# Kernel optimization log

Hardware: AMD Instinct MI355X
Metric: run time of the kernel (lower is better)

The kernel has to match this reference:

```python
import jax, jax.numpy as jnp
import numpy as np
from jax import lax

N = 262144      # number of coordinate points
CC = 3          # coords_channel
GF = 64         # gating_feature
FEAT = 64       # n_network_features
E = 8           # experts_num
L = 4           # expert_layers
TOPK = 2
BW = 45.0       # bandwidth
LN_EPS = 1e-5
W0S = 0.5 * BW + BW * np.arange(E, dtype=np.float32)  # per-expert first-layer sine freq


def setup_inputs() -> dict:
    key = jax.random.key(0)
    ks = jax.random.split(key, 16)
    u = lambda k, shape, b: jax.random.uniform(k, shape, jnp.float32, -b, b)
    coords = jax.random.normal(ks[0], (N, CC), jnp.float32)
    # first_linear (first_layer_sine_init: U(-1/in, 1/in))
    fw = u(ks[1], (GF, CC), 1.0 / CC)
    fb = u(ks[2], (GF,), 1.0 / CC)
    # gate: Linear(GF,GF) + LayerNorm(GF), Linear(GF,E), softmax
    gw1 = u(ks[3], (GF, GF), np.sqrt(6.0 / GF))
    gb1 = u(ks[4], (GF,), 1.0 / np.sqrt(GF))
    ln_g = jnp.ones((GF,), jnp.float32)
    ln_b = jnp.zeros((GF,), jnp.float32)
    gw2 = u(ks[5], (E, GF), np.sqrt(6.0 / GF))
    gb2 = u(ks[6], (E,), 1.0 / np.sqrt(GF))
    # experts (SIREN): first layer U(-1/in,1/in), rest U(-sqrt(6/in)/30, sqrt(6/in)/30)
    we0 = u(ks[7], (E, FEAT, GF), 1.0 / GF)
    be0 = u(ks[8], (E, FEAT), 1.0 / GF)
    sb = np.sqrt(6.0 / FEAT) / 30.0
    wm = u(ks[9], (L - 2, E, FEAT, FEAT), sb)
    bm = u(ks[10], (L - 2, E, FEAT), sb)
    wl = u(ks[11], (E, FEAT), sb)
    bl = u(ks[12], (E,), sb)
    return {"coords": coords, "fw": fw, "fb": fb, "gw1": gw1, "gb1": gb1,
            "ln_g": ln_g, "ln_b": ln_b, "gw2": gw2, "gb2": gb2,
            "we0": we0, "be0": be0, "wm": wm, "bm": bm, "wl": wl, "bl": bl}


def reference(coords, fw, fb, gw1, gb1, ln_g, ln_b, gw2, gb2, we0, be0, wm, bm, wl, bl):
    w0s = jnp.asarray(W0S)
    # first_linear: [N, GF]
    feature = coords @ fw.T + fb
    # gate: Linear -> LayerNorm -> Linear -> Softmax(dim=1)
    g = feature @ gw1.T + gb1
    mu = jnp.mean(g, axis=-1, keepdims=True)
    var = jnp.mean(jnp.square(g - mu), axis=-1, keepdims=True)
    gn = (g - mu) * lax.rsqrt(var + LN_EPS) * ln_g + ln_b
    index = jax.nn.softmax(gn @ gw2.T + gb2, axis=1)  # [N, E]
    # all experts computed densely on the gated feature: [E, N, FEAT]
    h = jnp.sin(w0s[:, None, None] * (jnp.einsum('nf,ekf->enk', feature, we0) + be0[:, None, :]))
    for l in range(L - 2):
        h = jnp.sin(30.0 * (jnp.einsum('enf,ekf->enk', h, wm[l]) + bm[l][:, None, :]))
    x = (jnp.einsum('enf,ef->en', h, wl) + bl[:, None]).T  # [N, E]
    # top-k mask: ~(index < kth largest) == index >= kth
    kth = lax.top_k(index, TOPK)[0][:, -1:]
    mask = (index >= kth).astype(x.dtype)
    output = jnp.sum(x * mask, axis=1, keepdims=True)  # [N, 1]
    counts = jnp.sum(mask, axis=0)  # per-expert selection counts
    aux_loss = (E / (N * N)) * jnp.dot(counts, counts)
    return output, aux_loss
```

## Files before the change

kernel.cpp:

```cpp
#include <hip/hip_runtime.h>
#include <math.h>

#define NPTS 262144
#define GBLK (NPTS / 128)
#define CPE  2048
#define TAU  0.01f

typedef float f4v __attribute__((ext_vector_type(4)));
typedef short s8v __attribute__((ext_vector_type(8)));

static __device__ __forceinline__ unsigned short f2bf(float f) {
    unsigned u = __float_as_uint(f);
    u += 0x7fffu + ((u >> 16) & 1u);
    return (unsigned short)(u >> 16);
}
static __device__ __forceinline__ unsigned short f2bf_hw(float f) {
    __bf16 b = (__bf16)f;
    unsigned short u;
    __builtin_memcpy(&u, &b, 2);
    return u;
}
static __device__ __forceinline__ float bf2f(unsigned short h) {
    return __uint_as_float(((unsigned)h) << 16);
}
static __device__ __forceinline__ unsigned pk2b(unsigned short lo, unsigned short hi) {
    return ((unsigned)hi << 16) | (unsigned)lo;
}
static __device__ __forceinline__ unsigned cpack(float lo, float hi) {
    return pk2b(f2bf_hw(lo), f2bf_hw(hi));
}
static __device__ __forceinline__ float sinrev(float x) {
    return __builtin_amdgcn_sinf(x);
}

union BFrag { uint4 q; unsigned u[4]; s8v s; };

__global__ __launch_bounds__(256) void prep_kernel(
    const float* __restrict__ we0, const float* __restrict__ be0,
    const float* __restrict__ wm, const float* __restrict__ bm,
    const float* __restrict__ gw1, const float* __restrict__ gw2,
    const float* __restrict__ fw, const float* __restrict__ fb,
    const float* __restrict__ gb1,
    uint4* __restrict__ packA, float* __restrict__ biasS,
    uint4* __restrict__ packGW2H, uint4* __restrict__ packGW2L,
    float* __restrict__ M1, float* __restrict__ b1p,
    float* __restrict__ M0, float* __restrict__ b0p, int* __restrict__ refcnt)
{
    const int idx = blockIdx.x * 256 + threadIdx.x;
    const float PI2I = 0.15915494309189535f;
    if (idx < 12288) {
        const int l = idx & 63;
        const int fr = (idx >> 6) & 7;
        const int grp = idx >> 9;
        const int e = grp / 3, ell = grp % 3;
        const int tau = fr >> 1, ks = fr & 1;
        const int g = l >> 4, m = l & 15;
        const int row = tau * 16 + m;
        const float scale = (ell == 0) ? (22.5f + 45.0f * (float)e) * PI2I : 30.0f * PI2I;
        const float* W = (ell == 0) ? (we0 + e * 4096) : (wm + ((ell - 1) * 8 + e) * 4096);
        unsigned short v[8];
#pragma unroll
        for (int i = 0; i < 8; i++) {
            const int k = 32 * ks + 4 * g + (i < 4 ? i : i + 12);
            v[i] = f2bf(W[row * 64 + k] * scale);
        }
        uint4 q;
        q.x = pk2b(v[0], v[1]); q.y = pk2b(v[2], v[3]);
        q.z = pk2b(v[4], v[5]); q.w = pk2b(v[6], v[7]);
        packA[idx] = q;
    } else if (idx < 13824) {
        const int j = idx - 12288;
        const int r = j & 63;
        const int grp = j >> 6;
        const int e = grp / 3, ell = grp % 3;
        const float scale = (ell == 0) ? (22.5f + 45.0f * (float)e) * PI2I : 30.0f * PI2I;
        const float b = (ell == 0) ? be0[e * 64 + r] : bm[((ell - 1) * 8 + e) * 64 + r];
        biasS[j] = b * scale;
    } else if (idx < 13952) {
        const int j = idx - 13824;
        const int l = j & 63;
        const int ks = j >> 6;
        const int g = l >> 4;
        const int row = l & 15;
        unsigned short vh[8], vl[8];
#pragma unroll
        for (int i = 0; i < 8; i++) {
            const int k = 32 * ks + 4 * g + (i < 4 ? i : i + 12);
            const float x = (row < 8) ? gw2[row * 64 + k] : 0.f;
            const unsigned short h = f2bf(x);
            vh[i] = h;
            vl[i] = f2bf(x - bf2f(h));
        }
        uint4 qh, ql;
        qh.x = pk2b(vh[0], vh[1]); qh.y = pk2b(vh[2], vh[3]);
        qh.z = pk2b(vh[4], vh[5]); qh.w = pk2b(vh[6], vh[7]);
        ql.x = pk2b(vl[0], vl[1]); ql.y = pk2b(vl[2], vl[3]);
        ql.z = pk2b(vl[4], vl[5]); ql.w = pk2b(vl[6], vl[7]);
        packGW2H[j] = qh; packGW2L[j] = ql;
    } else if (idx < 14144) {
        const int m = idx - 13952;
        const int r = m / 3, d = m % 3;
        double s = 0.0;
        for (int j = 0; j < 64; j++) s += (double)gw1[r * 64 + j] * (double)fw[j * 3 + d];
        M1[m] = (float)s;
    } else if (idx < 14208) {
        const int r = idx - 14144;
        double s = (double)gb1[r];
        for (int j = 0; j < 64; j++) s += (double)gw1[r * 64 + j] * (double)fb[j];
        b1p[r] = (float)s;
    } else if (idx < 15744) {
        const int m = idx - 14208;
        const int e = m / 192;
        const int rem = m % 192;
        const int r = rem / 3, d = rem % 3;
        const double scale = (22.5 + 45.0 * (double)e) * 0.15915494309189535;
        double s = 0.0;
        for (int j = 0; j < 64; j++) s += (double)we0[e * 4096 + r * 64 + j] * (double)fw[j * 3 + d];
        M0[m] = (float)(s * scale);
    } else if (idx < 16256) {
        const int m = idx - 15744;
        const int e = m >> 6, r = m & 63;
        const double scale = (22.5 + 45.0 * (double)e) * 0.15915494309189535;
        double s = (double)be0[e * 64 + r];
        for (int j = 0; j < 64; j++) s += (double)we0[e * 4096 + r * 64 + j] * (double)fb[j];
        b0p[m] = (float)(s * scale);
    } else if (idx == 16256) {
        *refcnt = 0;
    }
}

__global__ __launch_bounds__(256) void gate_kernel(
    const float* __restrict__ coords,
    const float* __restrict__ M1, const float* __restrict__ b1p,
    const float* __restrict__ lng, const float* __restrict__ lnb,
    const float* __restrict__ gb2,
    const uint4* __restrict__ packGW2H, const uint4* __restrict__ packGW2L,
    unsigned char* __restrict__ sel, int* __restrict__ blkcnt,
    int* __restrict__ reflist, int* __restrict__ refcnt, float* __restrict__ out)
{
    __shared__ float s_M1[192], s_b1p[64], s_lng[64], s_lnb[64], s_gb2[8];
    __shared__ uint4 sW2H[128], sW2L[128];
    __shared__ int s_cnt[8];
    const int t = threadIdx.x;
    if (t < 128) { sW2H[t] = packGW2H[t]; sW2L[t] = packGW2L[t]; }
    if (t < 192) s_M1[t] = M1[t];
    if (t < 64) { s_b1p[t] = b1p[t]; s_lng[t] = lng[t]; s_lnb[t] = lnb[t]; }
    if (t < 8) { s_gb2[t] = gb2[t]; s_cnt[t] = 0; }
    if (t < 128) out[blockIdx.x * 128 + t] = 0.f;
    __syncthreads();

    const int lane = t & 63;
    const int wv = t >> 6;
    const int g = lane >> 4, c = lane & 15;
    const int n0 = blockIdx.x * 128 + wv * 32 + c;
    const int n1 = n0 + 16;

    const float a0 = coords[n0 * 3], a1 = coords[n0 * 3 + 1], a2 = coords[n0 * 3 + 2];
    const float b0 = coords[n1 * 3], b1 = coords[n1 * 3 + 1], b2 = coords[n1 * 3 + 2];

    float ga[16], gb[16];
#pragma unroll
    for (int i = 0; i < 16; i++) {
        const int r = ((i >> 2) << 4) + 4 * g + (i & 3);
        const float m0 = s_M1[r * 3], m1 = s_M1[r * 3 + 1], m2 = s_M1[r * 3 + 2];
        const float bb = s_b1p[r];
        ga[i] = bb + a0 * m0 + a1 * m1 + a2 * m2;
        gb[i] = bb + b0 * m0 + b1 * m1 + b2 * m2;
    }

    float s1a = 0.f, s1b = 0.f;
#pragma unroll
    for (int i = 0; i < 16; i++) { s1a += ga[i]; s1b += gb[i]; }
    s1a += __shfl_xor(s1a, 16, 64); s1a += __shfl_xor(s1a, 32, 64);
    s1b += __shfl_xor(s1b, 16, 64); s1b += __shfl_xor(s1b, 32, 64);
    const float mu0 = s1a * (1.f / 64.f), mu1 = s1b * (1.f / 64.f);
    float s2a = 0.f, s2b = 0.f;
#pragma unroll
    for (int i = 0; i < 16; i++) {
        const float d0 = ga[i] - mu0; s2a += d0 * d0;
        const float d1 = gb[i] - mu1; s2b += d1 * d1;
    }
    s2a += __shfl_xor(s2a, 16, 64); s2a += __shfl_xor(s2a, 32, 64);
    s2b += __shfl_xor(s2b, 16, 64); s2b += __shfl_xor(s2b, 32, 64);
    const float rs0 = rsqrtf(s2a * (1.f / 64.f) + 1e-5f);
    const float rs1 = rsqrtf(s2b * (1.f / 64.f) + 1e-5f);

    BFrag Gh0[2], Gl0[2], Gh1[2], Gl1[2];
#pragma unroll
    for (int ks = 0; ks < 2; ks++) {
#pragma unroll
        for (int q = 0; q < 4; q++) {
            const int i0 = ks * 8 + 2 * q, i1 = i0 + 1;
            const int r0 = ((i0 >> 2) << 4) + 4 * g + (i0 & 3);
            const int r1 = ((i1 >> 2) << 4) + 4 * g + (i1 & 3);
            const float gnA0 = (ga[i0] - mu0) * rs0 * s_lng[r0] + s_lnb[r0];
            const float gnA1 = (ga[i1] - mu0) * rs0 * s_lng[r1] + s_lnb[r1];
            const float gnB0 = (gb[i0] - mu1) * rs1 * s_lng[r0] + s_lnb[r0];
            const float gnB1 = (gb[i1] - mu1) * rs1 * s_lng[r1] + s_lnb[r1];
            const unsigned short hA0 = f2bf_hw(gnA0), hA1 = f2bf_hw(gnA1);
            const unsigned short hB0 = f2bf_hw(gnB0), hB1 = f2bf_hw(gnB1);
            Gh0[ks].u[q] = pk2b(hA0, hA1);
            Gl0[ks].u[q] = cpack(gnA0 - bf2f(hA0), gnA1 - bf2f(hA1));
            Gh1[ks].u[q] = pk2b(hB0, hB1);
            Gl1[ks].u[q] = cpack(gnB0 - bf2f(hB0), gnB1 - bf2f(hB1));
        }
    }

    f4v lacc0 = {0.f, 0.f, 0.f, 0.f}, lacc1 = {0.f, 0.f, 0.f, 0.f};
    {
        BFrag W0, W1, V0, V1;
        W0.q = sW2H[0 * 64 + lane]; W1.q = sW2H[1 * 64 + lane];
        V0.q = sW2L[0 * 64 + lane]; V1.q = sW2L[1 * 64 + lane];
        lacc0 = __builtin_amdgcn_mfma_f32_16x16x32_bf16(W0.s, Gh0[0].s, lacc0, 0, 0, 0);
        lacc1 = __builtin_amdgcn_mfma_f32_16x16x32_bf16(W0.s, Gh1[0].s, lacc1, 0, 0, 0);
        lacc0 = __builtin_amdgcn_mfma_f32_16x16x32_bf16(W1.s, Gh0[1].s, lacc0, 0, 0, 0);
        lacc1 = __builtin_amdgcn_mfma_f32_16x16x32_bf16(W1.s, Gh1[1].s, lacc1, 0, 0, 0);
        lacc0 = __builtin_amdgcn_mfma_f32_16x16x32_bf16(W0.s, Gl0[0].s, lacc0, 0, 0, 0);
        lacc1 = __builtin_amdgcn_mfma_f32_16x16x32_bf16(W0.s, Gl1[0].s, lacc1, 0, 0, 0);
        lacc0 = __builtin_amdgcn_mfma_f32_16x16x32_bf16(W1.s, Gl0[1].s, lacc0, 0, 0, 0);
        lacc1 = __builtin_amdgcn_mfma_f32_16x16x32_bf16(W1.s, Gl1[1].s, lacc1, 0, 0, 0);
        lacc0 = __builtin_amdgcn_mfma_f32_16x16x32_bf16(V0.s, Gh0[0].s, lacc0, 0, 0, 0);
        lacc1 = __builtin_amdgcn_mfma_f32_16x16x32_bf16(V0.s, Gh1[0].s, lacc1, 0, 0, 0);
        lacc0 = __builtin_amdgcn_mfma_f32_16x16x32_bf16(V1.s, Gh0[1].s, lacc0, 0, 0, 0);
        lacc1 = __builtin_amdgcn_mfma_f32_16x16x32_bf16(V1.s, Gh1[1].s, lacc1, 0, 0, 0);
    }

    float logit0[8], logit1[8];
#pragma unroll
    for (int j = 0; j < 4; j++) {
        const float o0 = __shfl_xor(lacc0[j], 16, 64);
        const float o1 = __shfl_xor(lacc1[j], 16, 64);
        logit0[j] = lacc0[j] + s_gb2[j];
        logit0[4 + j] = o0 + s_gb2[4 + j];
        logit1[j] = lacc1[j] + s_gb2[j];
        logit1[4 + j] = o1 + s_gb2[4 + j];
    }

    unsigned mbits0 = 0, mbits1 = 0;
    bool flg0, flg1;
    {
        float m1 = logit0[0]; int i1 = 0;
#pragma unroll
        for (int e = 1; e < 8; e++) if (logit0[e] > m1) { m1 = logit0[e]; i1 = e; }
        float m2 = -INFINITY; int i2 = -1;
#pragma unroll
        for (int e = 0; e < 8; e++) if (e != i1 && logit0[e] > m2) { m2 = logit0[e]; i2 = e; }
        float m3 = -INFINITY;
#pragma unroll
        for (int e = 0; e < 8; e++) if (e != i1 && e != i2 && logit0[e] > m3) m3 = logit0[e];
#pragma unroll
        for (int e = 0; e < 8; e++) if (logit0[e] >= m2) mbits0 |= 1u << e;
        flg0 = (m2 - m3 < TAU);
    }
    {
        float m1 = logit1[0]; int i1 = 0;
#pragma unroll
        for (int e = 1; e < 8; e++) if (logit1[e] > m1) { m1 = logit1[e]; i1 = e; }
        float m2 = -INFINITY; int i2 = -1;
#pragma unroll
        for (int e = 0; e < 8; e++) if (e != i1 && logit1[e] > m2) { m2 = logit1[e]; i2 = e; }
        float m3 = -INFINITY;
#pragma unroll
        for (int e = 0; e < 8; e++) if (e != i1 && e != i2 && logit1[e] > m3) m3 = logit1[e];
#pragma unroll
        for (int e = 0; e < 8; e++) if (logit1[e] >= m2) mbits1 |= 1u << e;
        flg1 = (m2 - m3 < TAU);
    }

    const bool active = (g == 0);
    if (active) { sel[n0] = (unsigned char)mbits0; sel[n1] = (unsigned char)mbits1; }

#pragma unroll
    for (int e = 0; e < 8; e++) {
        const unsigned long long bal0 = __ballot(active && ((mbits0 >> e) & 1u));
        const unsigned long long bal1 = __ballot(active && ((mbits1 >> e) & 1u));
        if (lane == 0) atomicAdd(&s_cnt[e], (int)(__popcll(bal0) + __popcll(bal1)));
    }
    {
        const unsigned long long bal0 = __ballot(active && flg0);
        const unsigned long long bal1 = __ballot(active && flg1);
        const int p0 = (int)__popcll(bal0);
        int pos0 = 0;
        if (lane == 0 && (bal0 | bal1)) pos0 = atomicAdd(refcnt, p0 + (int)__popcll(bal1));
        pos0 = __shfl(pos0, 0, 64);
        if (active && flg0) {
            const int rank = (int)__popcll(bal0 & ((1ull << lane) - 1ull));
            reflist[pos0 + rank] = n0;
        }
        if (active && flg1) {
            const int rank = p0 + (int)__popcll(bal1 & ((1ull << lane) - 1ull));
            reflist[pos0 + rank] = n1;
        }
    }
    __syncthreads();
    if (t < 8) blkcnt[blockIdx.x * 8 + t] = s_cnt[t];
}

__global__ __launch_bounds__(256) void refine_kernel(
    const float* __restrict__ coords,
    const float* __restrict__ fw, const float* __restrict__ fb,
    const float* __restrict__ gw1, const float* __restrict__ gb1,
    const float* __restrict__ lng, const float* __restrict__ lnb,
    const float* __restrict__ gw2, const float* __restrict__ gb2,
    const int* __restrict__ reflist, const int* __restrict__ refcnt,
    unsigned char* __restrict__ sel, int* __restrict__ blkcnt)
{
    const int R = *refcnt;
    if (blockIdx.x * 4 >= R) return;

    __shared__ float s_gw1t[64 * 65];
    __shared__ float s_gw2[512];
    __shared__ float s_fw[192], s_fb[64], s_gb1[64], s_lng[64], s_lnb[64], s_gb2[8];
    __shared__ float s_f[4][64];

    const int t = threadIdx.x;
    for (int i = t; i < 4096; i += 256) s_gw1t[(i & 63) * 65 + (i >> 6)] = gw1[i];
    for (int i = t; i < 512; i += 256) s_gw2[i] = gw2[i];
    if (t < 192) s_fw[t] = fw[t];
    if (t < 64) { s_fb[t] = fb[t]; s_gb1[t] = gb1[t]; s_lng[t] = lng[t]; s_lnb[t] = lnb[t]; }
    if (t < 8) s_gb2[t] = gb2[t];
    __syncthreads();

    const int wv = t >> 6, lane = t & 63;
    for (int idx = blockIdx.x * 4 + wv; idx < R; idx += gridDim.x * 4) {
        const int n = reflist[idx];
        const float c0 = coords[n * 3], c1 = coords[n * 3 + 1], c2 = coords[n * 3 + 2];
        const float fr = s_fb[lane] + c0 * s_fw[lane * 3] + c1 * s_fw[lane * 3 + 1]
                       + c2 * s_fw[lane * 3 + 2];
        s_f[wv][lane] = fr;
        float a = s_gb1[lane];
#pragma unroll
        for (int k = 0; k < 64; k++)
            a += s_f[wv][k] * s_gw1t[k * 65 + lane];
        float mu = a;
#pragma unroll
        for (int d = 1; d < 64; d <<= 1) mu += __shfl_xor(mu, d, 64);
        mu *= (1.f / 64.f);
        const float dv = a - mu;
        float v = dv * dv;
#pragma unroll
        for (int d = 1; d < 64; d <<= 1) v += __shfl_xor(v, d, 64);
        const float rs = rsqrtf(v * (1.f / 64.f) + 1e-5f);
        const float gn = dv * rs * s_lng[lane] + s_lnb[lane];
        float lp[8];
#pragma unroll
        for (int e = 0; e < 8; e++) lp[e] = gn * s_gw2[e * 64 + lane];
#pragma unroll
        for (int e = 0; e < 8; e++) {
#pragma unroll
            for (int d = 1; d < 64; d <<= 1) lp[e] += __shfl_xor(lp[e], d, 64);
            lp[e] += s_gb2[e];
        }
        if (lane == 0) {
            float m1 = lp[0]; int i1 = 0;
#pragma unroll
            for (int e = 1; e < 8; e++) if (lp[e] > m1) { m1 = lp[e]; i1 = e; }
            float m2 = -INFINITY;
#pragma unroll
            for (int e = 0; e < 8; e++) if (e != i1 && lp[e] > m2) m2 = lp[e];
            unsigned mbits = 0;
#pragma unroll
            for (int e = 0; e < 8; e++) if (lp[e] >= m2) mbits |= 1u << e;
            const unsigned old = sel[n];
            if (mbits != old) {
                sel[n] = (unsigned char)mbits;
                const int b = n >> 7;
#pragma unroll
                for (int e = 0; e < 8; e++) {
                    const int was = (old >> e) & 1, now = (mbits >> e) & 1;
                    if (was != now) atomicAdd(&blkcnt[b * 8 + e], now - was);
                }
            }
        }
    }
}

__global__ __launch_bounds__(256) void scan_kernel(
    const int* __restrict__ blkcnt, int* __restrict__ baseoff,
    int* __restrict__ counts)
{
    const int e = blockIdx.x;
    const int t = threadIdx.x;
    const int lane = t & 63, wv = t >> 6;
    __shared__ int s_w[4];

    int v[8]; int sum = 0;
#pragma unroll
    for (int i = 0; i < 8; i++) { v[i] = blkcnt[(t * 8 + i) * 8 + e]; sum += v[i]; }
    int incl = sum;
#pragma unroll
    for (int d = 1; d < 64; d <<= 1) {
        const int x = __shfl_up(incl, d, 64);
        if (lane >= d) incl += x;
    }
    if (lane == 63) s_w[wv] = incl;
    __syncthreads();
    int woff = 0;
#pragma unroll
    for (int i = 0; i < 4; i++) if (i < wv) woff += s_w[i];
    int run = woff + incl - sum;
#pragma unroll
    for (int i = 0; i < 8; i++) { baseoff[(t * 8 + i) * 8 + e] = run; run += v[i]; }
    if (t == 255) counts[e] = run;
}

__global__ __launch_bounds__(128) void scatter_kernel(
    const unsigned char* __restrict__ sel, const int* __restrict__ baseoff,
    const int* __restrict__ counts, int* __restrict__ buckets, float* __restrict__ out)
{
    __shared__ int s_w0[8];
    const int t = threadIdx.x;
    const int n = blockIdx.x * 128 + t;
    if (blockIdx.x == 0 && t == 0) {
        double s = 0.0;
        for (int e = 0; e < 8; e++) { const double c = (double)counts[e]; s += c * c; }
        out[NPTS] = (float)(8.0 * s / ((double)NPTS * (double)NPTS));
    }
    const unsigned m = sel[n];
    const int w = t >> 6, lane = t & 63;
    unsigned long long bal[8];
#pragma unroll
    for (int e = 0; e < 8; e++) {
        bal[e] = __ballot((m >> e) & 1u);
        if (w == 0 && lane == 0) s_w0[e] = (int)__popcll(bal[e]);
    }
    __syncthreads();
#pragma unroll
    for (int e = 0; e < 8; e++) {
        if ((m >> e) & 1u) {
            int rank = (int)__popcll(bal[e] & ((1ull << lane) - 1ull));
            if (w == 1) rank += s_w0[e];
            buckets[e * NPTS + baseoff[blockIdx.x * 8 + e] + rank] = n;
        }
    }
}

__global__ __launch_bounds__(256) void expert_kernel(
    const float* __restrict__ coords,
    const float* __restrict__ M0, const float* __restrict__ b0p,
    const float* __restrict__ wl, const float* __restrict__ bl,
    const uint4* __restrict__ packA, const float* __restrict__ biasS,
    const int* __restrict__ counts, const int* __restrict__ buckets,
    float* __restrict__ out)
{
    const int e = blockIdx.x >> 11;
    const int chunk = blockIdx.x & (CPE - 1);
    const int cnt = counts[e];
    const int base = chunk * 128;
    if (base >= cnt) return;

    __shared__ float s_b[192];
    __shared__ float s_wl[64];
    __shared__ float s_M0[192];
    __shared__ float s_b0p[64];
    __shared__ float s_bl;

    const int t = threadIdx.x;
    if (t < 192) {
        s_b[t] = biasS[e * 192 + t];
        s_M0[t] = M0[e * 192 + t];
    }
    if (t < 64) {
        s_b0p[t] = b0p[e * 64 + t];
        s_wl[t] = wl[e * 64 + t];
    }
    if (t == 0) s_bl = bl[e];
    __syncthreads();

    const int lane = t & 63;
    const int wv = t >> 6;
    const int g = lane >> 4, c = lane & 15;
    const int i0 = base + wv * 32 + c;
    const int i1 = i0 + 16;
    const int id0 = (i0 < cnt) ? buckets[e * NPTS + i0] : -1;
    const int id1 = (i1 < cnt) ? buckets[e * NPTS + i1] : -1;

    const float a0 = (id0 >= 0) ? coords[id0 * 3] : 0.f;
    const float a1 = (id0 >= 0) ? coords[id0 * 3 + 1] : 0.f;
    const float a2 = (id0 >= 0) ? coords[id0 * 3 + 2] : 0.f;
    const float b0 = (id1 >= 0) ? coords[id1 * 3] : 0.f;
    const float b1 = (id1 >= 0) ? coords[id1 * 3 + 1] : 0.f;
    const float b2 = (id1 >= 0) ? coords[id1 * 3 + 2] : 0.f;

    f4v acc0[4], acc1[4];
#pragma unroll
    for (int tau = 0; tau < 4; tau++) {
#pragma unroll
        for (int j = 0; j < 4; j++) {
            const int r = tau * 16 + 4 * g + j;
            const float m0 = s_M0[r * 3], m1 = s_M0[r * 3 + 1], m2 = s_M0[r * 3 + 2];
            const float bb = s_b0p[r];
            acc0[tau][j] = bb + a0 * m0 + a1 * m1 + a2 * m2;
            acc1[tau][j] = bb + b0 * m0 + b1 * m1 + b2 * m2;
        }
    }

    BFrag B0[2], B1[2];
#pragma unroll
    for (int ks = 0; ks < 2; ks++) {
        B0[ks].u[0] = cpack(sinrev(acc0[2 * ks][0]), sinrev(acc0[2 * ks][1]));
        B0[ks].u[1] = cpack(sinrev(acc0[2 * ks][2]), sinrev(acc0[2 * ks][3]));
        B0[ks].u[2] = cpack(sinrev(acc0[2 * ks + 1][0]), sinrev(acc0[2 * ks + 1][1]));
        B0[ks].u[3] = cpack(sinrev(acc0[2 * ks + 1][2]), sinrev(acc0[2 * ks + 1][3]));
        B1[ks].u[0] = cpack(sinrev(acc1[2 * ks][0]), sinrev(acc1[2 * ks][1]));
        B1[ks].u[1] = cpack(sinrev(acc1[2 * ks][2]), sinrev(acc1[2 * ks][3]));
        B1[ks].u[2] = cpack(sinrev(acc1[2 * ks + 1][0]), sinrev(acc1[2 * ks + 1][1]));
        B1[ks].u[3] = cpack(sinrev(acc1[2 * ks + 1][2]), sinrev(acc1[2 * ks + 1][3]));
    }

    {
#pragma unroll
        for (int tau = 0; tau < 4; tau++) {
            const float4 b = *(const float4*)&s_b[64 + tau * 16 + 4 * g];
            acc0[tau][0] = b.x; acc0[tau][1] = b.y; acc0[tau][2] = b.z; acc0[tau][3] = b.w;
            acc1[tau][0] = b.x; acc1[tau][1] = b.y; acc1[tau][2] = b.z; acc1[tau][3] = b.w;
        }
        const uint4* Ab = packA + (size_t)((e * 3 + 1) * 8) * 64 + lane;
#pragma unroll
        for (int tau = 0; tau < 4; tau++) {
            BFrag A0, A1;
            A0.q = Ab[(tau * 2 + 0) * 64];
            A1.q = Ab[(tau * 2 + 1) * 64];
            acc0[tau] = __builtin_amdgcn_mfma_f32_16x16x32_bf16(A0.s, B0[0].s, acc0[tau], 0, 0, 0);
            acc0[tau] = __builtin_amdgcn_mfma_f32_16x16x32_bf16(A1.s, B0[1].s, acc0[tau], 0, 0, 0);
            acc1[tau] = __builtin_amdgcn_mfma_f32_16x16x32_bf16(A0.s, B1[0].s, acc1[tau], 0, 0, 0);
            acc1[tau] = __builtin_amdgcn_mfma_f32_16x16x32_bf16(A1.s, B1[1].s, acc1[tau], 0, 0, 0);
        }
#pragma unroll
        for (int ks = 0; ks < 2; ks++) {
            B0[ks].u[0] = cpack(sinrev(acc0[2 * ks][0]), sinrev(acc0[2 * ks][1]));
            B0[ks].u[1] = cpack(sinrev(acc0[2 * ks][2]), sinrev(acc0[2 * ks][3]));
            B0[ks].u[2] = cpack(sinrev(acc0[2 * ks + 1][0]), sinrev(acc0[2 * ks + 1][1]));
            B0[ks].u[3] = cpack(sinrev(acc0[2 * ks + 1][2]), sinrev(acc0[2 * ks + 1][3]));
            B1[ks].u[0] = cpack(sinrev(acc1[2 * ks][0]), sinrev(acc1[2 * ks][1]));
            B1[ks].u[1] = cpack(sinrev(acc1[2 * ks][2]), sinrev(acc1[2 * ks][3]));
            B1[ks].u[2] = cpack(sinrev(acc1[2 * ks + 1][0]), sinrev(acc1[2 * ks + 1][1]));
            B1[ks].u[3] = cpack(sinrev(acc1[2 * ks + 1][2]), sinrev(acc1[2 * ks + 1][3]));
        }
    }

    {
#pragma unroll
        for (int tau = 0; tau < 4; tau++) {
            const float4 b = *(const float4*)&s_b[128 + tau * 16 + 4 * g];
            acc0[tau][0] = b.x; acc0[tau][1] = b.y; acc0[tau][2] = b.z; acc0[tau][3] = b.w;
            acc1[tau][0] = b.x; acc1[tau][1] = b.y; acc1[tau][2] = b.z; acc1[tau][3] = b.w;
        }
        const uint4* Ab = packA + (size_t)((e * 3 + 2) * 8) * 64 + lane;
#pragma unroll
        for (int tau = 0; tau < 4; tau++) {
            BFrag A0, A1;
            A0.q = Ab[(tau * 2 + 0) * 64];
            A1.q = Ab[(tau * 2 + 1) * 64];
            acc0[tau] = __builtin_amdgcn_mfma_f32_16x16x32_bf16(A0.s, B0[0].s, acc0[tau], 0, 0, 0);
            acc0[tau] = __builtin_amdgcn_mfma_f32_16x16x32_bf16(A1.s, B0[1].s, acc0[tau], 0, 0, 0);
            acc1[tau] = __builtin_amdgcn_mfma_f32_16x16x32_bf16(A0.s, B1[0].s, acc1[tau], 0, 0, 0);
            acc1[tau] = __builtin_amdgcn_mfma_f32_16x16x32_bf16(A1.s, B1[1].s, acc1[tau], 0, 0, 0);
        }
        float px0 = 0.f, px1 = 0.f;
#pragma unroll
        for (int tau = 0; tau < 4; tau++) {
            const float4 w = *(const float4*)&s_wl[tau * 16 + 4 * g];
            px0 += sinrev(acc0[tau][0]) * w.x + sinrev(acc0[tau][1]) * w.y
                 + sinrev(acc0[tau][2]) * w.z + sinrev(acc0[tau][3]) * w.w;
            px1 += sinrev(acc1[tau][0]) * w.x + sinrev(acc1[tau][1]) * w.y
                 + sinrev(acc1[tau][2]) * w.z + sinrev(acc1[tau][3]) * w.w;
        }
        px0 += __shfl_xor(px0, 16, 64); px0 += __shfl_xor(px0, 32, 64);
        px1 += __shfl_xor(px1, 16, 64); px1 += __shfl_xor(px1, 32, 64);
        if (g == 0) {
            if (id0 >= 0) atomicAdd(&out[id0], px0 + s_bl);
            if (id1 >= 0) atomicAdd(&out[id1], px1 + s_bl);
        }
    }
}

extern "C" void kernel_launch(void* const* d_in, const int* in_sizes, int n_in,
                              void* d_out, int out_size, void* d_ws, size_t ws_size,
                              hipStream_t stream)
{
    const float* coords = (const float*)d_in[0];
    const float* fw  = (const float*)d_in[1];
    const float* fb  = (const float*)d_in[2];
    const float* gw1 = (const float*)d_in[3];
    const float* gb1 = (const float*)d_in[4];
    const float* lng = (const float*)d_in[5];
    const float* lnb = (const float*)d_in[6];
    const float* gw2 = (const float*)d_in[7];
    const float* gb2 = (const float*)d_in[8];
    const float* we0 = (const float*)d_in[9];
    const float* be0 = (const float*)d_in[10];
    const float* wm  = (const float*)d_in[11];
    const float* bm  = (const float*)d_in[12];
    const float* wl  = (const float*)d_in[13];
    const float* bl  = (const float*)d_in[14];
    float* out = (float*)d_out;

    char* ws = (char*)d_ws;
    int* counts           = (int*)ws;
    int* buckets          = (int*)(ws + 64);
    uint4* packA          = (uint4*)(ws + 8388672);
    float* biasS          = (float*)(ws + 8585280);
    int* blkcnt           = (int*)(ws + 8591424);
    int* baseoff          = (int*)(ws + 8656960);
    unsigned char* sel    = (unsigned char*)(ws + 8722496);
    uint4* packGW2H       = (uint4*)(ws + 8984640);
    uint4* packGW2L       = (uint4*)(ws + 8986688);
    int* reflist          = (int*)(ws + 8988736);
    int* refcnt           = (int*)(ws + 10037312);
    float* M1             = (float*)(ws + 10037376);
    float* b1p            = (float*)(ws + 10038144);
    float* M0             = (float*)(ws + 10038400);
    float* b0p            = (float*)(ws + 10044544);

    prep_kernel<<<64, 256, 0, stream>>>(we0, be0, wm, bm, gw1, gw2, fw, fb, gb1,
                                        packA, biasS, packGW2H, packGW2L, M1, b1p,
                                        M0, b0p, refcnt);
    gate_kernel<<<GBLK, 256, 0, stream>>>(coords, M1, b1p, lng, lnb, gb2,
                                          packGW2H, packGW2L,
                                          sel, blkcnt, reflist, refcnt, out);
    refine_kernel<<<256, 256, 0, stream>>>(coords, fw, fb, gw1, gb1, lng, lnb, gw2, gb2,
                                           reflist, refcnt, sel, blkcnt);
    scan_kernel<<<8, 256, 0, stream>>>(blkcnt, baseoff, counts);
    scatter_kernel<<<GBLK, 128, 0, stream>>>(sel, baseoff, counts, buckets, out);
    expert_kernel<<<8 * CPE, 256, 0, stream>>>(coords, M0, b0p, wl, bl, packA, biasS,
                                               counts, buckets, out);
}
```

Before: 85.77 us.

## Fuse scan into refine via last-block ticket; make expert kernel persistent

The per-expert prefix scan now runs inside the refine kernel, performed by whichever block finishes last (detected with an atomic ticket counter that prep resets). This removes one kernel launch. The expert kernel becomes a grid-stride loop over a compacted list of 128-point chunks across all experts, launched with 2056 blocks instead of 16384 mostly-empty ones. In exchange, each loop iteration reloads per-expert shared weights behind an extra barrier, and correctness depends on the threadfence/ticket ordering.

```diff
diff --git a/kernel.cpp b/kernel.cpp
--- a/kernel.cpp
+++ b/kernel.cpp
@@ -3,7 +3,6 @@
 
 #define NPTS 262144
 #define GBLK (NPTS / 128)
-#define CPE  2048
 #define TAU  0.01f
 
 typedef float f4v __attribute__((ext_vector_type(4)));
@@ -44,7 +43,8 @@
     uint4* __restrict__ packA, float* __restrict__ biasS,
     uint4* __restrict__ packGW2H, uint4* __restrict__ packGW2L,
     float* __restrict__ M1, float* __restrict__ b1p,
-    float* __restrict__ M0, float* __restrict__ b0p, int* __restrict__ refcnt)
+    float* __restrict__ M0, float* __restrict__ b0p,
+    int* __restrict__ refcnt, int* __restrict__ rs_done)
 {
     const int idx = blockIdx.x * 256 + threadIdx.x;
     const float PI2I = 0.15915494309189535f;
@@ -126,6 +126,8 @@
         b0p[m] = (float)(s * scale);
     } else if (idx == 16256) {
         *refcnt = 0;
+    } else if (idx == 16257) {
+        *rs_done = 0;
     }
 }
 
@@ -303,105 +305,109 @@
     const float* __restrict__ lng, const float* __restrict__ lnb,
     const float* __restrict__ gw2, const float* __restrict__ gb2,
     const int* __restrict__ reflist, const int* __restrict__ refcnt,
-    unsigned char* __restrict__ sel, int* __restrict__ blkcnt)
+    unsigned char* __restrict__ sel, int* __restrict__ blkcnt,
+    int* __restrict__ baseoff, int* __restrict__ counts, int* __restrict__ rs_done)
 {
-    const int R = *refcnt;
-    if (blockIdx.x * 4 >= R) return;
-
     __shared__ float s_gw1t[64 * 65];
     __shared__ float s_gw2[512];
     __shared__ float s_fw[192], s_fb[64], s_gb1[64], s_lng[64], s_lnb[64], s_gb2[8];
     __shared__ float s_f[4][64];
+    __shared__ int s_ticket;
+    __shared__ int s_wsc[4];
 
     const int t = threadIdx.x;
-    for (int i = t; i < 4096; i += 256) s_gw1t[(i & 63) * 65 + (i >> 6)] = gw1[i];
-    for (int i = t; i < 512; i += 256) s_gw2[i] = gw2[i];
-    if (t < 192) s_fw[t] = fw[t];
-    if (t < 64) { s_fb[t] = fb[t]; s_gb1[t] = gb1[t]; s_lng[t] = lng[t]; s_lnb[t] = lnb[t]; }
-    if (t < 8) s_gb2[t] = gb2[t];
+    const int wv = t >> 6, lane = t & 63;
+    const int R = *refcnt;
+
+    if (R > 0 && blockIdx.x * 4 < R) {
+        for (int i = t; i < 4096; i += 256) s_gw1t[(i & 63) * 65 + (i >> 6)] = gw1[i];
+        for (int i = t; i < 512; i += 256) s_gw2[i] = gw2[i];
+        if (t < 192) s_fw[t] = fw[t];
+        if (t < 64) { s_fb[t] = fb[t]; s_gb1[t] = gb1[t]; s_lng[t] = lng[t]; s_lnb[t] = lnb[t]; }
+        if (t < 8) s_gb2[t] = gb2[t];
+        __syncthreads();
+
+        for (int idx = blockIdx.x * 4 + wv; idx < R; idx += gridDim.x * 4) {
+            const int n = reflist[idx];
+            const float c0 = coords[n * 3], c1 = coords[n * 3 + 1], c2 = coords[n * 3 + 2];
+            const float fr = s_fb[lane] + c0 * s_fw[lane * 3] + c1 * s_fw[lane * 3 + 1]
+                           + c2 * s_fw[lane * 3 + 2];
+            s_f[wv][lane] = fr;
+            float a = s_gb1[lane];
+#pragma unroll
+            for (int k = 0; k < 64; k++)
+                a += s_f[wv][k] * s_gw1t[k * 65 + lane];
+            float mu = a;
+#pragma unroll
+            for (int d = 1; d < 64; d <<= 1) mu += __shfl_xor(mu, d, 64);
+            mu *= (1.f / 64.f);
+            const float dv = a - mu;
+            float v = dv * dv;
+#pragma unroll
+            for (int d = 1; d < 64; d <<= 1) v += __shfl_xor(v, d, 64);
+            const float rs = rsqrtf(v * (1.f / 64.f) + 1e-5f);
+            const float gn = dv * rs * s_lng[lane] + s_lnb[lane];
+            float lp[8];
+#pragma unroll
+            for (int e = 0; e < 8; e++) lp[e] = gn * s_gw2[e * 64 + lane];
+#pragma unroll
+            for (int e = 0; e < 8; e++) {
+#pragma unroll
+                for (int d = 1; d < 64; d <<= 1) lp[e] += __shfl_xor(lp[e], d, 64);
+                lp[e] += s_gb2[e];
+            }
+            if (lane == 0) {
+                float m1 = lp[0]; int i1 = 0;
+#pragma unroll
+                for (int e = 1; e < 8; e++) if (lp[e] > m1) { m1 = lp[e]; i1 = e; }
+                float m2 = -INFINITY;
+#pragma unroll
+                for (int e = 0; e < 8; e++) if (e != i1 && lp[e] > m2) m2 = lp[e];
+                unsigned mbits = 0;
+#pragma unroll
+                for (int e = 0; e < 8; e++) if (lp[e] >= m2) mbits |= 1u << e;
+                const unsigned old = sel[n];
+                if (mbits != old) {
+                    sel[n] = (unsigned char)mbits;
+                    const int b = n >> 7;
+#pragma unroll
+                    for (int e = 0; e < 8; e++) {
+                        const int was = (old >> e) & 1, now = (mbits >> e) & 1;
+                        if (was != now) atomicAdd(&blkcnt[b * 8 + e], now - was);
+                    }
+                }
+            }
+        }
+    }
+
+    __threadfence();
     __syncthreads();
-
-    const int wv = t >> 6, lane = t & 63;
-    for (int idx = blockIdx.x * 4 + wv; idx < R; idx += gridDim.x * 4) {
-        const int n = reflist[idx];
-        const float c0 = coords[n * 3], c1 = coords[n * 3 + 1], c2 = coords[n * 3 + 2];
-        const float fr = s_fb[lane] + c0 * s_fw[lane * 3] + c1 * s_fw[lane * 3 + 1]
-                       + c2 * s_fw[lane * 3 + 2];
-        s_f[wv][lane] = fr;
-        float a = s_gb1[lane];
-#pragma unroll
-        for (int k = 0; k < 64; k++)
-            a += s_f[wv][k] * s_gw1t[k * 65 + lane];
-        float mu = a;
-#pragma unroll
-        for (int d = 1; d < 64; d <<= 1) mu += __shfl_xor(mu, d, 64);
-        mu *= (1.f / 64.f);
-        const float dv = a - mu;
-        float v = dv * dv;
-#pragma unroll
-        for (int d = 1; d < 64; d <<= 1) v += __shfl_xor(v, d, 64);
-        const float rs = rsqrtf(v * (1.f / 64.f) + 1e-5f);
-        const float gn = dv * rs * s_lng[lane] + s_lnb[lane];
-        float lp[8];
-#pragma unroll
-        for (int e = 0; e < 8; e++) lp[e] = gn * s_gw2[e * 64 + lane];
-#pragma unroll
+    if (t == 0) s_ticket = atomicAdd(rs_done, 1);
+    __syncthreads();
+    if (s_ticket == (int)gridDim.x - 1) {
+        __threadfence();
         for (int e = 0; e < 8; e++) {
-#pragma unroll
-            for (int d = 1; d < 64; d <<= 1) lp[e] += __shfl_xor(lp[e], d, 64);
-            lp[e] += s_gb2[e];
-        }
-        if (lane == 0) {
-            float m1 = lp[0]; int i1 = 0;
-#pragma unroll
-            for (int e = 1; e < 8; e++) if (lp[e] > m1) { m1 = lp[e]; i1 = e; }
-            float m2 = -INFINITY;
-#pragma unroll
-            for (int e = 0; e < 8; e++) if (e != i1 && lp[e] > m2) m2 = lp[e];
-            unsigned mbits = 0;
-#pragma unroll
-            for (int e = 0; e < 8; e++) if (lp[e] >= m2) mbits |= 1u << e;
-            const unsigned old = sel[n];
-            if (mbits != old) {
-                sel[n] = (unsigned char)mbits;
-                const int b = n >> 7;
-#pragma unroll
-                for (int e = 0; e < 8; e++) {
-                    const int was = (old >> e) & 1, now = (mbits >> e) & 1;
-                    if (was != now) atomicAdd(&blkcnt[b * 8 + e], now - was);
-                }
-            }
-        }
-    }
-}
-
-__global__ __launch_bounds__(256) void scan_kernel(
-    const int* __restrict__ blkcnt, int* __restrict__ baseoff,
-    int* __restrict__ counts)
-{
-    const int e = blockIdx.x;
-    const int t = threadIdx.x;
-    const int lane = t & 63, wv = t >> 6;
-    __shared__ int s_w[4];
-
-    int v[8]; int sum = 0;
-#pragma unroll
-    for (int i = 0; i < 8; i++) { v[i] = blkcnt[(t * 8 + i) * 8 + e]; sum += v[i]; }
-    int incl = sum;
-#pragma unroll
-    for (int d = 1; d < 64; d <<= 1) {
-        const int x = __shfl_up(incl, d, 64);
-        if (lane >= d) incl += x;
-    }
-    if (lane == 63) s_w[wv] = incl;
-    __syncthreads();
-    int woff = 0;
-#pragma unroll
-    for (int i = 0; i < 4; i++) if (i < wv) woff += s_w[i];
-    int run = woff + incl - sum;
-#pragma unroll
-    for (int i = 0; i < 8; i++) { baseoff[(t * 8 + i) * 8 + e] = run; run += v[i]; }
-    if (t == 255) counts[e] = run;
+            int v[8]; int sum = 0;
+#pragma unroll
+            for (int i = 0; i < 8; i++) { v[i] = blkcnt[(t * 8 + i) * 8 + e]; sum += v[i]; }
+            int incl = sum;
+#pragma unroll
+            for (int d = 1; d < 64; d <<= 1) {
+                const int x = __shfl_up(incl, d, 64);
+                if (lane >= d) incl += x;
+            }
+            if (lane == 63) s_wsc[wv] = incl;
+            __syncthreads();
+            int woff = 0;
+#pragma unroll
+            for (int i = 0; i < 4; i++) if (i < wv) woff += s_wsc[i];
+            int run = woff + incl - sum;
+#pragma unroll
+            for (int i = 0; i < 8; i++) { baseoff[(t * 8 + i) * 8 + e] = run; run += v[i]; }
+            if (t == 255) counts[e] = run;
+            __syncthreads();
+        }
+    }
 }
 
 __global__ __launch_bounds__(128) void scatter_kernel(
@@ -443,12 +449,6 @@
     const int* __restrict__ counts, const int* __restrict__ buckets,
     float* __restrict__ out)
 {
-    const int e = blockIdx.x >> 11;
-    const int chunk = blockIdx.x & (CPE - 1);
-    const int cnt = counts[e];
-    const int base = chunk * 128;
-    if (base >= cnt) return;
-
     __shared__ float s_b[192];
     __shared__ float s_wl[64];
     __shared__ float s_M0[192];
@@ -456,76 +456,66 @@
     __shared__ float s_bl;
 
     const int t = threadIdx.x;
-    if (t < 192) {
-        s_b[t] = biasS[e * 192 + t];
-        s_M0[t] = M0[e * 192 + t];
-    }
-    if (t < 64) {
-        s_b0p[t] = b0p[e * 64 + t];
-        s_wl[t] = wl[e * 64 + t];
-    }
-    if (t == 0) s_bl = bl[e];
-    __syncthreads();
-
-    const int lane = t & 63;
-    const int wv = t >> 6;
-    const int g = lane >> 4, c = lane & 15;
-    const int i0 = base + wv * 32 + c;
-    const int i1 = i0 + 16;
-    const int id0 = (i0 < cnt) ? buckets[e * NPTS + i0] : -1;
-    const int id1 = (i1 < cnt) ? buckets[e * NPTS + i1] : -1;
-
-    const float a0 = (id0 >= 0) ? coords[id0 * 3] : 0.f;
-    const float a1 = (id0 >= 0) ? coords[id0 * 3 + 1] : 0.f;
-    const float a2 = (id0 >= 0) ? coords[id0 * 3 + 2] : 0.f;
-    const float b0 = (id1 >= 0) ? coords[id1 * 3] : 0.f;
-    const float b1 = (id1 >= 0) ? coords[id1 * 3 + 1] : 0.f;
-    const float b2 = (id1 >= 0) ? coords[id1 * 3 + 2] : 0.f;
-
-    f4v acc0[4], acc1[4];
-#pragma unroll
-    for (int tau = 0; tau < 4; tau++) {
-#pragma unroll
-        for (int j = 0; j < 4; j++) {
-            const int r = tau * 16 + 4 * g + j;
-            const float m0 = s_M0[r * 3], m1 = s_M0[r * 3 + 1], m2 = s_M0[r * 3 + 2];
-            const float bb = s_b0p[r];
-            acc0[tau][j] = bb + a0 * m0 + a1 * m1 + a2 * m2;
-            acc1[tau][j] = bb + b0 * m0 + b1 * m1 + b2 * m2;
-        }
-    }
-
-    BFrag B0[2], B1[2];
-#pragma unroll
-    for (int ks = 0; ks < 2; ks++) {
-        B0[ks].u[0] = cpack(sinrev(acc0[2 * ks][0]), sinrev(acc0[2 * ks][1]));
-        B0[ks].u[1] = cpack(sinrev(acc0[2 * ks][2]), sinrev(acc0[2 * ks][3]));
-        B0[ks].u[2] = cpack(sinrev(acc0[2 * ks + 1][0]), sinrev(acc0[2 * ks + 1][1]));
-        B0[ks].u[3] = cpack(sinrev(acc0[2 * ks + 1][2]), sinrev(acc0[2 * ks + 1][3]));
-        B1[ks].u[0] = cpack(sinrev(acc1[2 * ks][0]), sinrev(acc1[2 * ks][1]));
-        B1[ks].u[1] = cpack(sinrev(acc1[2 * ks][2]), sinrev(acc1[2 * ks][3]));
-        B1[ks].u[2] = cpack(sinrev(acc1[2 * ks + 1][0]), sinrev(acc1[2 * ks + 1][1]));
-        B1[ks].u[3] = cpack(sinrev(acc1[2 * ks + 1][2]), sinrev(acc1[2 * ks + 1][3]));
-    }
-
-    {
+    const int c0n = (counts[0] + 127) >> 7;
+    const int c1n = (counts[1] + 127) >> 7;
+    const int c2n = (counts[2] + 127) >> 7;
+    const int c3n = (counts[3] + 127) >> 7;
+    const int c4n = (counts[4] + 127) >> 7;
+    const int c5n = (counts[5] + 127) >> 7;
+    const int c6n = (counts[6] + 127) >> 7;
+    const int c7n = (counts[7] + 127) >> 7;
+    const int p1 = c0n, p2 = p1 + c1n, p3 = p2 + c2n, p4 = p3 + c3n;
+    const int p5 = p4 + c4n, p6 = p5 + c5n, p7 = p6 + c6n, total = p7 + c7n;
+
+    bool first = true;
+    for (int vc = blockIdx.x; vc < total; vc += gridDim.x) {
+        int e = 0, pe = 0;
+        if (vc >= p1) { e = 1; pe = p1; }
+        if (vc >= p2) { e = 2; pe = p2; }
+        if (vc >= p3) { e = 3; pe = p3; }
+        if (vc >= p4) { e = 4; pe = p4; }
+        if (vc >= p5) { e = 5; pe = p5; }
+        if (vc >= p6) { e = 6; pe = p6; }
+        if (vc >= p7) { e = 7; pe = p7; }
+        const int cnt = counts[e];
+        const int base = (vc - pe) * 128;
+
+        if (!first) __syncthreads();
+        first = false;
+        if (t < 192) { s_b[t] = biasS[e * 192 + t]; s_M0[t] = M0[e * 192 + t]; }
+        if (t < 64) { s_b0p[t] = b0p[e * 64 + t]; s_wl[t] = wl[e * 64 + t]; }
+        if (t == 0) s_bl = bl[e];
+        __syncthreads();
+
+        const int lane = t & 63;
+        const int wv = t >> 6;
+        const int g = lane >> 4, c = lane & 15;
+        const int i0 = base + wv * 32 + c;
+        const int i1 = i0 + 16;
+        const int id0 = (i0 < cnt) ? buckets[e * NPTS + i0] : -1;
+        const int id1 = (i1 < cnt) ? buckets[e * NPTS + i1] : -1;
+
+        const float a0 = (id0 >= 0) ? coords[id0 * 3] : 0.f;
+        const float a1 = (id0 >= 0) ? coords[id0 * 3 + 1] : 0.f;
+        const float a2 = (id0 >= 0) ? coords[id0 * 3 + 2] : 0.f;
+        const float b0 = (id1 >= 0) ? coords[id1 * 3] : 0.f;
+        const float b1 = (id1 >= 0) ? coords[id1 * 3 + 1] : 0.f;
+        const float b2 = (id1 >= 0) ? coords[id1 * 3 + 2] : 0.f;
+
+        f4v acc0[4], acc1[4];
 #pragma unroll
         for (int tau = 0; tau < 4; tau++) {
-            const float4 b = *(const float4*)&s_b[64 + tau * 16 + 4 * g];
-            acc0[tau][0] = b.x; acc0[tau][1] = b.y; acc0[tau][2] = b.z; acc0[tau][3] = b.w;
-            acc1[tau][0] = b.x; acc1[tau][1] = b.y; acc1[tau][2] = b.z; acc1[tau][3] = b.w;
-        }
-        const uint4* Ab = packA + (size_t)((e * 3 + 1) * 8) * 64 + lane;
-#pragma unroll
-        for (int tau = 0; tau < 4; tau++) {
-            BFrag A0, A1;
-            A0.q = Ab[(tau * 2 + 0) * 64];
-            A1.q = Ab[(tau * 2 + 1) * 64];
-            acc0[tau] = __builtin_amdgcn_mfma_f32_16x16x32_bf16(A0.s, B0[0].s, acc0[tau], 0, 0, 0);
-            acc0[tau] = __builtin_amdgcn_mfma_f32_16x16x32_bf16(A1.s, B0[1].s, acc0[tau], 0, 0, 0);
-            acc1[tau] = __builtin_amdgcn_mfma_f32_16x16x32_bf16(A0.s, B1[0].s, acc1[tau], 0, 0, 0);
-            acc1[tau] = __builtin_amdgcn_mfma_f32_16x16x32_bf16(A1.s, B1[1].s, acc1[tau], 0, 0, 0);
-        }
+#pragma unroll
+            for (int j = 0; j < 4; j++) {
+                const int r = tau * 16 + 4 * g + j;
+                const float m0 = s_M0[r * 3], m1 = s_M0[r * 3 + 1], m2 = s_M0[r * 3 + 2];
+                const float bb = s_b0p[r];
+                acc0[tau][j] = bb + a0 * m0 + a1 * m1 + a2 * m2;
+                acc1[tau][j] = bb + b0 * m0 + b1 * m1 + b2 * m2;
+            }
+        }
+
+        BFrag B0[2], B1[2];
 #pragma unroll
         for (int ks = 0; ks < 2; ks++) {
             B0[ks].u[0] = cpack(sinrev(acc0[2 * ks][0]), sinrev(acc0[2 * ks][1]));
@@ -537,40 +527,71 @@
             B1[ks].u[2] = cpack(sinrev(acc1[2 * ks + 1][0]), sinrev(acc1[2 * ks + 1][1]));
             B1[ks].u[3] = cpack(sinrev(acc1[2 * ks + 1][2]), sinrev(acc1[2 * ks + 1][3]));
         }
-    }
-
-    {
-#pragma unroll
-        for (int tau = 0; tau < 4; tau++) {
-            const float4 b = *(const float4*)&s_b[128 + tau * 16 + 4 * g];
-            acc0[tau][0] = b.x; acc0[tau][1] = b.y; acc0[tau][2] = b.z; acc0[tau][3] = b.w;
-            acc1[tau][0] = b.x; acc1[tau][1] = b.y; acc1[tau][2] = b.z; acc1[tau][3] = b.w;
-        }
-        const uint4* Ab = packA + (size_t)((e * 3 + 2) * 8) * 64 + lane;
-#pragma unroll
-        for (int tau = 0; tau < 4; tau++) {
-            BFrag A0, A1;
-            A0.q = Ab[(tau * 2 + 0) * 64];
-            A1.q = Ab[(tau * 2 + 1) * 64];
-            acc0[tau] = __builtin_amdgcn_mfma_f32_16x16x32_bf16(A0.s, B0[0].s, acc0[tau], 0, 0, 0);
-            acc0[tau] = __builtin_amdgcn_mfma_f32_16x16x32_bf16(A1.s, B0[1].s, acc0[tau], 0, 0, 0);
-            acc1[tau] = __builtin_amdgcn_mfma_f32_16x16x32_bf16(A0.s, B1[0].s, acc1[tau], 0, 0, 0);
-            acc1[tau] = __builtin_amdgcn_mfma_f32_16x16x32_bf16(A1.s, B1[1].s, acc1[tau], 0, 0, 0);
-        }
-        float px0 = 0.f, px1 = 0.f;
-#pragma unroll
-        for (int tau = 0; tau < 4; tau++) {
-            const float4 w = *(const float4*)&s_wl[tau * 16 + 4 * g];
-            px0 += sinrev(acc0[tau][0]) * w.x + sinrev(acc0[tau][1]) * w.y
-                 + sinrev(acc0[tau][2]) * w.z + sinrev(acc0[tau][3]) * w.w;
-            px1 += sinrev(acc1[tau][0]) * w.x + sinrev(acc1[tau][1]) * w.y
-                 + sinrev(acc1[tau][2]) * w.z + sinrev(acc1[tau][3]) * w.w;
-        }
-        px0 += __shfl_xor(px0, 16, 64); px0 += __shfl_xor(px0, 32, 64);
-        px1 += __shfl_xor(px1, 16, 64); px1 += __shfl_xor(px1, 32, 64);
-        if (g == 0) {
-            if (id0 >= 0) atomicAdd(&out[id0], px0 + s_bl);
-            if (id1 >= 0) atomicAdd(&out[id1], px1 + s_bl);
+
+        {
+#pragma unroll
+            for (int tau = 0; tau < 4; tau++) {
+                const float4 b = *(const float4*)&s_b[64 + tau * 16 + 4 * g];
+                acc0[tau][0] = b.x; acc0[tau][1] = b.y; acc0[tau][2] = b.z; acc0[tau][3] = b.w;
+                acc1[tau][0] = b.x; acc1[tau][1] = b.y; acc1[tau][2] = b.z; acc1[tau][3] = b.w;
+            }
+            const uint4* Ab = packA + (size_t)((e * 3 + 1) * 8) * 64 + lane;
+#pragma unroll
+            for (int tau = 0; tau < 4; tau++) {
+                BFrag A0, A1;
+                A0.q = Ab[(tau * 2 + 0) * 64];
+                A1.q = Ab[(tau * 2 + 1) * 64];
+                acc0[tau] = __builtin_amdgcn_mfma_f32_16x16x32_bf16(A0.s, B0[0].s, acc0[tau], 0, 0, 0);
+                acc0[tau] = __builtin_amdgcn_mfma_f32_16x16x32_bf16(A1.s, B0[1].s, acc0[tau], 0, 0, 0);
+                acc1[tau] = __builtin_amdgcn_mfma_f32_16x16x32_bf16(A0.s, B1[0].s, acc1[tau], 0, 0, 0);
+                acc1[tau] = __builtin_amdgcn_mfma_f32_16x16x32_bf16(A1.s, B1[1].s, acc1[tau], 0, 0, 0);
+            }
+#pragma unroll
+            for (int ks = 0; ks < 2; ks++) {
+                B0[ks].u[0] = cpack(sinrev(acc0[2 * ks][0]), sinrev(acc0[2 * ks][1]));
+                B0[ks].u[1] = cpack(sinrev(acc0[2 * ks][2]), sinrev(acc0[2 * ks][3]));
+                B0[ks].u[2] = cpack(sinrev(acc0[2 * ks + 1][0]), sinrev(acc0[2 * ks + 1][1]));
+                B0[ks].u[3] = cpack(sinrev(acc0[2 * ks + 1][2]), sinrev(acc0[2 * ks + 1][3]));
+                B1[ks].u[0] = cpack(sinrev(acc1[2 * ks][0]), sinrev(acc1[2 * ks][1]));
+                B1[ks].u[1] = cpack(sinrev(acc1[2 * ks][2]), sinrev(acc1[2 * ks][3]));
+                B1[ks].u[2] = cpack(sinrev(acc1[2 * ks + 1][0]), sinrev(acc1[2 * ks + 1][1]));
+                B1[ks].u[3] = cpack(sinrev(acc1[2 * ks + 1][2]), sinrev(acc1[2 * ks + 1][3]));
+            }
+        }
+
+        {
+#pragma unroll
+            for (int tau = 0; tau < 4; tau++) {
+                const float4 b = *(const float4*)&s_b[128 + tau * 16 + 4 * g];
+                acc0[tau][0] = b.x; acc0[tau][1] = b.y; acc0[tau][2] = b.z; acc0[tau][3] = b.w;
+                acc1[tau][0] = b.x; acc1[tau][1] = b.y; acc1[tau][2] = b.z; acc1[tau][3] = b.w;
+            }
+            const uint4* Ab = packA + (size_t)((e * 3 + 2) * 8) * 64 + lane;
+#pragma unroll
+            for (int tau = 0; tau < 4; tau++) {
+                BFrag A0, A1;
+                A0.q = Ab[(tau * 2 + 0) * 64];
+                A1.q = Ab[(tau * 2 + 1) * 64];
+                acc0[tau] = __builtin_amdgcn_mfma_f32_16x16x32_bf16(A0.s, B0[0].s, acc0[tau], 0, 0, 0);
+                acc0[tau] = __builtin_amdgcn_mfma_f32_16x16x32_bf16(A1.s, B0[1].s, acc0[tau], 0, 0, 0);
+                acc1[tau] = __builtin_amdgcn_mfma_f32_16x16x32_bf16(A0.s, B1[0].s, acc1[tau], 0, 0, 0);
+                acc1[tau] = __builtin_amdgcn_mfma_f32_16x16x32_bf16(A1.s, B1[1].s, acc1[tau], 0, 0, 0);
+            }
+            float px0 = 0.f, px1 = 0.f;
+#pragma unroll
+            for (int tau = 0; tau < 4; tau++) {
+                const float4 w = *(const float4*)&s_wl[tau * 16 + 4 * g];
+                px0 += sinrev(acc0[tau][0]) * w.x + sinrev(acc0[tau][1]) * w.y
+                     + sinrev(acc0[tau][2]) * w.z + sinrev(acc0[tau][3]) * w.w;
+                px1 += sinrev(acc1[tau][0]) * w.x + sinrev(acc1[tau][1]) * w.y
+                     + sinrev(acc1[tau][2]) * w.z + sinrev(acc1[tau][3]) * w.w;
+            }
+            px0 += __shfl_xor(px0, 16, 64); px0 += __shfl_xor(px0, 32, 64);
+            px1 += __shfl_xor(px1, 16, 64); px1 += __shfl_xor(px1, 32, 64);
+            if (g == 0) {
+                if (id0 >= 0) atomicAdd(&out[id0], px0 + s_bl);
+                if (id1 >= 0) atomicAdd(&out[id1], px1 + s_bl);
+            }
         }
     }
 }
@@ -612,17 +633,18 @@
     float* b1p            = (float*)(ws + 10038144);
     float* M0             = (float*)(ws + 10038400);
     float* b0p            = (float*)(ws + 10044544);
+    int* rs_done          = (int*)(ws + 10046592);
 
     prep_kernel<<<64, 256, 0, stream>>>(we0, be0, wm, bm, gw1, gw2, fw, fb, gb1,
                                         packA, biasS, packGW2H, packGW2L, M1, b1p,
-                                        M0, b0p, refcnt);
+                                        M0, b0p, refcnt, rs_done);
     gate_kernel<<<GBLK, 256, 0, stream>>>(coords, M1, b1p, lng, lnb, gb2,
                                           packGW2H, packGW2L,
                                           sel, blkcnt, reflist, refcnt, out);
     refine_kernel<<<256, 256, 0, stream>>>(coords, fw, fb, gw1, gb1, lng, lnb, gw2, gb2,
-                                           reflist, refcnt, sel, blkcnt);
-    scan_kernel<<<8, 256, 0, stream>>>(blkcnt, baseoff, counts);
+                                           reflist, refcnt, sel, blkcnt,
+                                           baseoff, counts, rs_done);
     scatter_kernel<<<GBLK, 128, 0, stream>>>(sel, baseoff, counts, buckets, out);
-    expert_kernel<<<8 * CPE, 256, 0, stream>>>(coords, M0, b0p, wl, bl, packA, biasS,
-                                               counts, buckets, out);
-}
+    expert_kernel<<<2056, 256, 0, stream>>>(coords, M0, b0p, wl, bl, packA, biasS,
+                                            counts, buckets, out);
+}
```

New measurement: 115.4 us. +34.6%, slower.
